# Optimization experiments

Measured on AMD Instinct MI355X. Metric: run time of the kernel, lower is better.

## Reference

```python
import jax, jax.numpy as jnp
import numpy as np

HIDDEN = 8192
K = 32
DIMS = [512, 768]
BATCH = 16384

def _xavier(key, shape):
    fan_out, fan_in = shape
    limit = np.sqrt(6.0 / (fan_in + fan_out)).astype(np.float32)
    return jax.random.uniform(key, shape, dtype=jnp.float32, minval=-limit, maxval=limit)

def setup_inputs() -> dict:
    key = jax.random.key(0)
    ks = jax.random.split(key, 6)
    return {
        "x0": jax.random.normal(ks[0], (BATCH, DIMS[0]), dtype=jnp.float32),
        "x1": jax.random.normal(ks[1], (BATCH, DIMS[1]), dtype=jnp.float32),
        "pre_bias0": jnp.zeros((DIMS[0],), dtype=jnp.float32),
        "pre_bias1": jnp.zeros((DIMS[1],), dtype=jnp.float32),
        "enc_w0": _xavier(ks[2], (HIDDEN, DIMS[0])),   # nn.Linear(d0, hidden).weight
        "enc_w1": _xavier(ks[3], (HIDDEN, DIMS[1])),
        "dec_w0": _xavier(ks[4], (DIMS[0], HIDDEN)),   # nn.Linear(hidden, d0).weight
        "dec_w1": _xavier(ks[5], (DIMS[1], HIDDEN)),
        "post_bias0": jnp.zeros((DIMS[0],), dtype=jnp.float32),
        "post_bias1": jnp.zeros((DIMS[1],), dtype=jnp.float32),
        "source_idx": 0,
    }

def _topk_sparse(z, k):
    # keep top-k per row, zero the rest (hard TopK activation)
    vals, idx = jax.lax.top_k(z, k)                      # [B, k]
    rows = jnp.arange(z.shape[0])[:, None]               # [B, 1]
    return jnp.zeros_like(z).at[rows, idx].set(vals)

def reference(x0, x1, pre_bias0, pre_bias1, enc_w0, enc_w1,
              dec_w0, dec_w1, post_bias0, post_bias1, source_idx):
    xs = (x0, x1)
    pbs = (pre_bias0, pre_bias1)
    ews = (enc_w0, enc_w1)
    # encode from source model: pre-bias subtract -> linear -> TopK sparsify
    x = xs[source_idx]
    z_dense = (x - pbs[source_idx]) @ ews[source_idx].T   # [B, HIDDEN]
    z = _topk_sparse(z_dense, K)
    # decode to every model's activation space
    rec0 = z @ dec_w0.T + post_bias0                      # [B, d0]
    rec1 = z @ dec_w1.T + post_bias1                      # [B, d1]
    return (z, rec0, rec1)
```

## Files before the change

kernel.cpp:

```cpp
#include <hip/hip_runtime.h>


#define BATCH  16384
#define HIDDEN 8192
#define DIM0   512
#define DIM1   768
#define TOPK   32
#define CAND_MAX 256
#define WIN_LO 36
#define WIN_HI 64

#define KLO_G 0xBECDu
#define KHI_G 0xC020u

typedef __attribute__((ext_vector_type(8))) short bf16x8;
typedef __attribute__((ext_vector_type(8))) unsigned short u16x8;
typedef __attribute__((ext_vector_type(4))) float f32x4;

__device__ __forceinline__ unsigned fkey(float f) {
    unsigned u = __float_as_uint(f);
    return (u & 0x80000000u) ? ~u : (u | 0x80000000u);
}
__device__ __forceinline__ unsigned fkey16(unsigned short h) {
    return (h & 0x8000u) ? (unsigned)((~h) & 0xFFFFu) : (unsigned)(h | 0x8000u);
}
__device__ __forceinline__ unsigned short f2b(float f) {
    unsigned u = __float_as_uint(f);
    unsigned r = (u + 0x7FFFu + ((u >> 16) & 1u)) >> 16;
    return (unsigned short)r;
}
__device__ __forceinline__ float b2f(unsigned short h) {
    return __uint_as_float(((unsigned)h) << 16);
}
__device__ __forceinline__ void load_lds16(const void* g, void* l) {
    __builtin_amdgcn_global_load_lds((const __attribute__((address_space(1))) void*)g,
                                     (__attribute__((address_space(3))) void*)l, 16, 0, 0);
}

template<int SRC>
__device__ __forceinline__ void convert_impl(
    const float* __restrict__ x, const float* __restrict__ pb,
    const float* __restrict__ w,
    unsigned short* __restrict__ xb, unsigned short* __restrict__ wb)
{
    constexpr int D = SRC ? DIM1 : DIM0;
    const int nx4 = BATCH * D / 4;
    const int nw4 = HIDDEN * D / 4;
    for (int i = blockIdx.x * blockDim.x + threadIdx.x; i < nx4 + nw4;
         i += gridDim.x * blockDim.x) {
        if (i < nx4) {
            float4 v = ((const float4*)x)[i];
            const int k = (i * 4) % D;
            v.x -= pb[k]; v.y -= pb[k + 1]; v.z -= pb[k + 2]; v.w -= pb[k + 3];
            ushort4 o; o.x = f2b(v.x); o.y = f2b(v.y); o.z = f2b(v.z); o.w = f2b(v.w);
            ((ushort4*)xb)[i] = o;
        } else {
            const float4 v = ((const float4*)w)[i - nx4];
            ushort4 o; o.x = f2b(v.x); o.y = f2b(v.y); o.z = f2b(v.z); o.w = f2b(v.w);
            ((ushort4*)wb)[i - nx4] = o;
        }
    }
}

__global__ void convert_xw(const float* __restrict__ x0, const float* __restrict__ x1,
                           const float* __restrict__ pb0, const float* __restrict__ pb1,
                           const float* __restrict__ w0, const float* __restrict__ w1,
                           const int* __restrict__ srcp,
                           unsigned short* __restrict__ xb, unsigned short* __restrict__ wb)
{
    if (*srcp == 0) convert_impl<0>(x0, pb0, w0, xb, wb);
    else            convert_impl<1>(x1, pb1, w1, xb, wb);
}

__global__ void transpose_dec_bf16(const float* __restrict__ dec,
                                   unsigned short* __restrict__ decT, int DD)
{
    __shared__ float t[32][33];
    const int hb = blockIdx.x * 32, db = blockIdx.y * 32;
    const int lx = threadIdx.x, ly = threadIdx.y;
#pragma unroll
    for (int s = 0; s < 32; s += 8)
        t[ly + s][lx] = dec[(size_t)(db + ly + s) * HIDDEN + hb + lx];
    __syncthreads();
#pragma unroll
    for (int s = 0; s < 32; s += 8)
        decT[(size_t)(hb + ly + s) * DD + db + lx] = f2b(t[lx][ly + s]);
}

template<int SRC>
__device__ __forceinline__ void gemm_impl(
    const unsigned short* __restrict__ xb, const unsigned short* __restrict__ wb,
    float* __restrict__ z, unsigned short* As, unsigned short* Bs)
{
    constexpr int D = SRC ? DIM1 : DIM0;

    const int nwg = gridDim.x;
    int id = blockIdx.x;
    id = (id & 7) * (nwg >> 3) + (id >> 3);
    const int bx = id & 63;
    const int by = id >> 6;
    const int m0 = by * 128, n0 = bx * 128;

    const int tid  = threadIdx.x;
    const int lane = tid & 63;
    const int wid  = tid >> 6;
    const int wr   = wid >> 1;
    const int wc   = wid & 1;
    const int l15  = lane & 15;
    const int g    = lane >> 4;

    f32x4 acc[4][4];
#pragma unroll
    for (int i = 0; i < 4; ++i)
#pragma unroll
        for (int j = 0; j < 4; ++j) acc[i][j] = (f32x4){0.f, 0.f, 0.f, 0.f};

    for (int k0 = 0; k0 < D; k0 += 64) {
#pragma unroll
        for (int q = 0; q < 4; ++q) {
            const int c   = wid * 256 + q * 64 + lane;
            const int row = c >> 3, jb = c & 7;
            const int j   = jb ^ (row & 7);
            load_lds16(xb + (size_t)(m0 + row) * D + k0 + j * 8,
                       As + (size_t)(wid * 256 + q * 64) * 8);
            load_lds16(wb + (size_t)(n0 + row) * D + k0 + j * 8,
                       Bs + (size_t)(wid * 256 + q * 64) * 8);
        }
        __syncthreads();

#pragma unroll
        for (int kk = 0; kk < 2; ++kk) {
            bf16x8 a[4], b[4];
#pragma unroll
            for (int f = 0; f < 4; ++f) {
                const int rA = wr * 64 + f * 16 + l15;
                const int sA = ((kk * 4 + g) ^ (rA & 7)) * 16;
                a[f] = *(const bf16x8*)((const char*)As + rA * 128 + sA);
                const int rB = wc * 64 + f * 16 + l15;
                const int sB = ((kk * 4 + g) ^ (rB & 7)) * 16;
                b[f] = *(const bf16x8*)((const char*)Bs + rB * 128 + sB);
            }
#pragma unroll
            for (int fi = 0; fi < 4; ++fi)
#pragma unroll
                for (int fj = 0; fj < 4; ++fj)
                    acc[fi][fj] = __builtin_amdgcn_mfma_f32_16x16x32_bf16(
                        a[fi], b[fj], acc[fi][fj], 0, 0, 0);
        }
        __syncthreads();
    }

#pragma unroll
    for (int fi = 0; fi < 4; ++fi) {
        const int row = m0 + wr * 64 + fi * 16 + g * 4;
#pragma unroll
        for (int fj = 0; fj < 4; ++fj) {
            const int col = n0 + wc * 64 + fj * 16 + l15;
#pragma unroll
            for (int r = 0; r < 4; ++r) {
                unsigned short* zs =
                    (unsigned short*)((char*)z + (size_t)(row + r) * (HIDDEN * 4));
                zs[col] = f2b(acc[fi][fj][r]);
            }
        }
    }

    if (bx >= 32) {
        const f32x4 zv = (f32x4){0.f, 0.f, 0.f, 0.f};
        const int c4 = (4096 >> 2) + (bx - 32) * 32 + (tid & 31);
#pragma unroll
        for (int pass = 0; pass < 16; ++pass) {
            const int r = m0 + pass * 8 + (tid >> 5);
            __builtin_nontemporal_store(zv, (f32x4*)(z + (size_t)r * HIDDEN) + c4);
        }
    }
}

__global__ __launch_bounds__(256, 2)
void gemm_bf16(const unsigned short* __restrict__ xb, const unsigned short* __restrict__ wb,
               const int* __restrict__ srcp, float* __restrict__ z)
{
    __shared__ unsigned short As[128 * 64];
    __shared__ unsigned short Bs[128 * 64];
    if (*srcp == 0) gemm_impl<0>(xb, wb, z, As, Bs);
    else            gemm_impl<1>(xb, wb, z, As, Bs);
}

template<int SRC>
__device__ __forceinline__ void topk_impl(
    float* __restrict__ z,
    const float* __restrict__ xsrc, const float* __restrict__ pb,
    const float* __restrict__ ew,
    const unsigned short* __restrict__ dTb0, const unsigned short* __restrict__ dTb1,
    const float* __restrict__ po0, const float* __restrict__ po1,
    float* __restrict__ rec0, float* __restrict__ rec1,
    float* xs, int* cidx, float* cval, unsigned char* cflag,
    int* counts, unsigned* pcounts, int* s_cnt, float* selv, int* seli)
{
    constexpr int D = SRC ? DIM1 : DIM0;

    const int tid = threadIdx.x;
    const size_t row = blockIdx.x;
    float* __restrict__ zrow = z + row * HIDDEN;
    const unsigned short* __restrict__ zsrow =
        (const unsigned short*)((const char*)z + row * (HIDDEN * 4));

    if (tid < D / 4) {
        const float4 xv = ((const float4*)(xsrc + row * D))[tid];
        const float4 pv = ((const float4*)pb)[tid];
        ((float4*)xs)[tid] = make_float4(xv.x - pv.x, xv.y - pv.y,
                                         xv.z - pv.z, xv.w - pv.w);
    }
    if (tid == 0) *s_cnt = 0;

    unsigned pkey[16];
#pragma unroll
    for (int s = 0; s < 4; ++s) {
        const u16x8 v = *(const u16x8*)(zsrow + (size_t)(s * 256 + tid) * 8);
#pragma unroll
        for (int p = 0; p < 4; ++p)
            pkey[s * 4 + p] = fkey16(v[2 * p]) | (fkey16(v[2 * p + 1]) << 16);
    }

    const f32x4 zv4 = (f32x4){0.f, 0.f, 0.f, 0.f};
#pragma unroll
    for (int s = 0; s < 4; ++s)
        __builtin_nontemporal_store(zv4, (f32x4*)&zrow[(size_t)(s * 256 + tid) * 4]);

    {
        int clo = 0, chi = 0;
#pragma unroll
        for (int p = 0; p < 16; ++p) {
            const unsigned klo16 = pkey[p] & 0xFFFFu, khi16 = pkey[p] >> 16;
            clo += (klo16 > KLO_G) ? 1 : 0;  chi += (klo16 > KHI_G) ? 1 : 0;
            clo += (khi16 > KLO_G) ? 1 : 0;  chi += (khi16 > KHI_G) ? 1 : 0;
        }
        unsigned pk = (unsigned)clo | ((unsigned)chi << 16);
#pragma unroll
        for (int off = 32; off; off >>= 1) pk += __shfl_xor(pk, off);
        if ((tid & 63) == 0) pcounts[tid >> 6] = pk;
    }
    __syncthreads();
    const unsigned ptot = pcounts[0] + pcounts[1] + pcounts[2] + pcounts[3];
    const int tot_lo = (int)(ptot & 0xFFFFu), tot_hi = (int)(ptot >> 16);

    unsigned kappa;
    int found = 0;
    if (tot_lo >= WIN_LO && tot_lo <= WIN_HI)      { kappa = KLO_G; found = 1; }
    else if (tot_hi >= WIN_LO && tot_hi <= WIN_HI) { kappa = KHI_G; found = 1; }
    if (!found) {
        unsigned lo = 0u, hi = 65535u;
        if (tot_lo > WIN_HI) lo = KLO_G;
        if (tot_lo < WIN_LO) hi = KLO_G;
        if (tot_hi > WIN_HI) lo = KHI_G;
        if (tot_hi < WIN_LO) hi = (hi < KHI_G) ? hi : KHI_G;
        kappa = lo;
        for (int it = 0; it < 18; ++it) {
            const unsigned mid = (lo + hi) >> 1;
            int c = 0;
#pragma unroll
            for (int p = 0; p < 16; ++p) {
                c += ((pkey[p] & 0xFFFFu) > mid) ? 1 : 0;
                c += ((pkey[p] >> 16)     > mid) ? 1 : 0;
            }
#pragma unroll
            for (int off = 32; off; off >>= 1) c += __shfl_xor(c, off);
            if ((tid & 63) == 0) counts[(it & 1) * 4 + (tid >> 6)] = c;
            __syncthreads();
            const int* cb = counts + (it & 1) * 4;
            const int tot = cb[0] + cb[1] + cb[2] + cb[3];
            if (tot >= WIN_LO && tot <= WIN_HI) { kappa = mid; break; }
            if (tot > WIN_HI) lo = mid; else hi = mid;
            kappa = lo;
            if (hi - lo <= 1u) break;
        }
    }

#pragma unroll
    for (int p = 0; p < 16; ++p) {
#pragma unroll
        for (int h = 0; h < 2; ++h) {
            const unsigned k16 = h ? (pkey[p] >> 16) : (pkey[p] & 0xFFFFu);
            if (k16 > kappa) {
                const int j = 2 * p + h;
                const int slot = atomicAdd(s_cnt, 1);
                if (slot < CAND_MAX)
                    cidx[slot] = ((j >> 3) * 256 + tid) * 8 + (j & 7);
            }
        }
    }
    __syncthreads();
    const int C = min(*s_cnt, CAND_MAX);

    {
        const int grp = tid >> 3, j8 = tid & 7;
        for (int c = grp; c < C; c += 32) {
            const float* __restrict__ wrow = ew + (size_t)cidx[c] * D;
            float4 a4 = make_float4(0.f, 0.f, 0.f, 0.f);
#pragma unroll
            for (int b = 0; b < D / 256; ++b) {
                float4 wv[8];
#pragma unroll
                for (int u = 0; u < 8; ++u)
                    wv[u] = *(const float4*)&wrow[b * 256 + u * 32 + j8 * 4];
#pragma unroll
                for (int u = 0; u < 8; ++u) {
                    const float4 x4 = *(const float4*)&xs[b * 256 + u * 32 + j8 * 4];
                    a4.x = fmaf(x4.x, wv[u].x, a4.x);
                    a4.y = fmaf(x4.y, wv[u].y, a4.y);
                    a4.z = fmaf(x4.z, wv[u].z, a4.z);
                    a4.w = fmaf(x4.w, wv[u].w, a4.w);
                }
            }
            float a = (a4.x + a4.y) + (a4.z + a4.w);
            a += __shfl_xor(a, 1);
            a += __shfl_xor(a, 2);
            a += __shfl_xor(a, 4);
            if (j8 == 0) cval[c] = a;
        }
    }
    __syncthreads();

    if (tid < C) {
        const float v = cval[tid];
        const int  ix = cidx[tid];
        int rank = 0;
        for (int j = 0; j < C; ++j) {
            const float vj = cval[j];
            rank += (vj > v || (vj == v && cidx[j] < ix)) ? 1 : 0;
        }
        cflag[tid] = (rank < TOPK) ? 1 : 0;
    }
    __syncthreads();
    if (tid < C && cflag[tid]) {
        const int ix = cidx[tid];
        int sr = 0;
        for (int j = 0; j < C; ++j) sr += (cflag[j] && cidx[j] < ix) ? 1 : 0;
        selv[sr] = cval[tid];
        seli[sr] = ix;
    }
    __syncthreads();

    if (tid < TOPK) zrow[seli[tid]] = selv[tid];

#pragma unroll
    for (int pass = 0; pass < 2; ++pass) {
        const int slot = pass * 256 + tid;
        if (slot < (DIM0 + DIM1) / 4) {
            const bool is0 = slot < DIM0 / 4;
            const int d0 = is0 ? slot * 4 : (slot - DIM0 / 4) * 4;
            const int DD = is0 ? DIM0 : DIM1;
            const unsigned short* __restrict__ dT = is0 ? dTb0 : dTb1;
            const float* __restrict__ po = is0 ? po0 : po1;
            f32x4 a;
            {
                const float4 p4 = *(const float4*)&po[d0];
                a = (f32x4){p4.x, p4.y, p4.z, p4.w};
            }
#pragma unroll
            for (int b = 0; b < TOPK / 8; ++b) {
                ushort4 wv[8];
#pragma unroll
                for (int u = 0; u < 8; ++u)
                    wv[u] = *(const ushort4*)&dT[(size_t)seli[b * 8 + u] * DD + d0];
#pragma unroll
                for (int u = 0; u < 8; ++u) {
                    const float sv = selv[b * 8 + u];
                    a.x = fmaf(sv, b2f(wv[u].x), a.x);
                    a.y = fmaf(sv, b2f(wv[u].y), a.y);
                    a.z = fmaf(sv, b2f(wv[u].z), a.z);
                    a.w = fmaf(sv, b2f(wv[u].w), a.w);
                }
            }
            float* __restrict__ out = is0 ? (rec0 + row * DIM0 + d0)
                                          : (rec1 + row * DIM1 + d0);
            __builtin_nontemporal_store(a, (f32x4*)out);
        }
    }
}

__global__ __launch_bounds__(256, 4)
void topk_rescore_decode(float* __restrict__ z,
                         const float* __restrict__ x0, const float* __restrict__ x1,
                         const float* __restrict__ pb0, const float* __restrict__ pb1,
                         const float* __restrict__ ew0, const float* __restrict__ ew1,
                         const unsigned short* __restrict__ dTb0,
                         const unsigned short* __restrict__ dTb1,
                         const float* __restrict__ po0, const float* __restrict__ po1,
                         float* __restrict__ rec0, float* __restrict__ rec1,
                         const int* __restrict__ srcp)
{
    __shared__ float         xs[DIM1];
    __shared__ int           cidx[CAND_MAX];
    __shared__ float         cval[CAND_MAX];
    __shared__ unsigned char cflag[CAND_MAX];
    __shared__ int           counts[2 * 4];
    __shared__ unsigned      pcounts[4];
    __shared__ int           s_cnt;
    __shared__ float         selv[TOPK];
    __shared__ int           seli[TOPK];

    if (*srcp == 0)
        topk_impl<0>(z, x0, pb0, ew0, dTb0, dTb1, po0, po1, rec0, rec1,
                     xs, cidx, cval, cflag, counts, pcounts, &s_cnt, selv, seli);
    else
        topk_impl<1>(z, x1, pb1, ew1, dTb0, dTb1, po0, po1, rec0, rec1,
                     xs, cidx, cval, cflag, counts, pcounts, &s_cnt, selv, seli);
}


__global__ __launch_bounds__(256, 2)
void encode_gemm(const float* __restrict__ x0, const float* __restrict__ x1,
                 const float* __restrict__ pb0, const float* __restrict__ pb1,
                 const float* __restrict__ w0, const float* __restrict__ w1,
                 const int* __restrict__ srcp, float* __restrict__ z)
{
    const int src = *srcp;
    const float* __restrict__ x  = (src == 0) ? x0 : x1;
    const float* __restrict__ pb = (src == 0) ? pb0 : pb1;
    const float* __restrict__ w  = (src == 0) ? w0 : w1;
    const int D = (src == 0) ? DIM0 : DIM1;

    __shared__ float As[16][132];
    __shared__ float Bs[16][132];

    const int tid = threadIdx.x;
    const int m0 = blockIdx.y * 128;
    const int n0 = blockIdx.x * 128;

    const int cA0 = tid,          cA1 = tid + 256;
    const int r0  = cA0 >> 2,     kq0 = (cA0 & 3) * 4;
    const int r1  = cA1 >> 2,     kq1 = (cA1 & 3) * 4;

    const int mf = (tid & 15) * 4;
    const int nf = (tid >> 4) * 4;

    float acc[8][8];
#pragma unroll
    for (int i = 0; i < 8; ++i)
#pragma unroll
        for (int j = 0; j < 8; ++j) acc[i][j] = 0.0f;

    for (int k0 = 0; k0 < D; k0 += 16) {
        const float4 av0 = *(const float4*)(x + (size_t)(m0 + r0) * D + k0 + kq0);
        const float4 av1 = *(const float4*)(x + (size_t)(m0 + r1) * D + k0 + kq1);
        const float4 pv0 = *(const float4*)(pb + k0 + kq0);
        const float4 pv1 = *(const float4*)(pb + k0 + kq1);
        const float4 bv0 = *(const float4*)(w + (size_t)(n0 + r0) * D + k0 + kq0);
        const float4 bv1 = *(const float4*)(w + (size_t)(n0 + r1) * D + k0 + kq1);
        As[kq0 + 0][r0] = av0.x - pv0.x;
        As[kq0 + 1][r0] = av0.y - pv0.y;
        As[kq0 + 2][r0] = av0.z - pv0.z;
        As[kq0 + 3][r0] = av0.w - pv0.w;
        As[kq1 + 0][r1] = av1.x - pv1.x;
        As[kq1 + 1][r1] = av1.y - pv1.y;
        As[kq1 + 2][r1] = av1.z - pv1.z;
        As[kq1 + 3][r1] = av1.w - pv1.w;
        Bs[kq0 + 0][r0] = bv0.x;
        Bs[kq0 + 1][r0] = bv0.y;
        Bs[kq0 + 2][r0] = bv0.z;
        Bs[kq0 + 3][r0] = bv0.w;
        Bs[kq1 + 0][r1] = bv1.x;
        Bs[kq1 + 1][r1] = bv1.y;
        Bs[kq1 + 2][r1] = bv1.z;
        Bs[kq1 + 3][r1] = bv1.w;
        __syncthreads();
#pragma unroll
        for (int kk = 0; kk < 16; ++kk) {
            const float4 A0 = *(const float4*)&As[kk][mf];
            const float4 A1 = *(const float4*)&As[kk][mf + 64];
            const float4 B0 = *(const float4*)&Bs[kk][nf];
            const float4 B1 = *(const float4*)&Bs[kk][nf + 64];
            const float a[8] = {A0.x, A0.y, A0.z, A0.w, A1.x, A1.y, A1.z, A1.w};
            const float b[8] = {B0.x, B0.y, B0.z, B0.w, B1.x, B1.y, B1.z, B1.w};
#pragma unroll
            for (int i = 0; i < 8; ++i)
#pragma unroll
                for (int j = 0; j < 8; ++j)
                    acc[i][j] = fmaf(a[i], b[j], acc[i][j]);
        }
        __syncthreads();
    }

#pragma unroll
    for (int i = 0; i < 8; ++i) {
        const int row = m0 + mf + (i & 3) + (i >> 2) * 64;
        const float4 v0 = make_float4(acc[i][0], acc[i][1], acc[i][2], acc[i][3]);
        const float4 v1 = make_float4(acc[i][4], acc[i][5], acc[i][6], acc[i][7]);
        *(float4*)(z + (size_t)row * HIDDEN + n0 + nf)      = v0;
        *(float4*)(z + (size_t)row * HIDDEN + n0 + nf + 64) = v1;
    }
}

__global__ __launch_bounds__(256, 2)
void topk_decode_fb(float* __restrict__ z,
                    const float* __restrict__ dA, const float* __restrict__ dB,
                    const float* __restrict__ po0, const float* __restrict__ po1,
                    float* __restrict__ rec0, float* __restrict__ rec1)
{
    __shared__ float    rowv[HIDDEN];
    __shared__ unsigned hist[4][257];
    __shared__ unsigned scanbuf[256];
    __shared__ float    selv[TOPK];
    __shared__ int      seli[TOPK];
    __shared__ unsigned sh_byte, sh_gt;

    const int tid = threadIdx.x;
    const size_t rowid = blockIdx.x;
    float* __restrict__ zrow = z + rowid * HIDDEN;

#pragma unroll
    for (int s = 0; s < 8; ++s) {
        const int i4 = s * 256 + tid;
        *(float4*)&rowv[i4 * 4] = *(const float4*)&zrow[i4 * 4];
    }
    __syncthreads();

    unsigned prefix = 0, prefmask = 0, need = TOPK;
#pragma unroll
    for (int p = 3; p >= 0; --p) {
        for (int i = tid; i < 4 * 257; i += 256) (&hist[0][0])[i] = 0;
        __syncthreads();
        const int sh = p * 8;
        for (int s = 0; s < 32; ++s) {
            const int i = s * 256 + tid;
            const unsigned k = fkey(rowv[i]);
            if ((k & prefmask) == prefix)
                atomicAdd(&hist[tid & 3][(k >> sh) & 255], 1);
        }
        __syncthreads();
        const unsigned tot = hist[0][tid] + hist[1][tid] + hist[2][tid] + hist[3][tid];
        hist[0][tid] = tot;
        __syncthreads();
        if (tid == 0) {
            unsigned cum = 0;
            int b = 255;
            for (;; --b) {
                const unsigned c = hist[0][b];
                if (cum + c >= need || b == 0) { sh_byte = (unsigned)b; sh_gt = cum; break; }
                cum += c;
            }
        }
        __syncthreads();
        prefix  |= sh_byte << sh;
        prefmask |= 0xFFu << sh;
        need -= sh_gt;
        __syncthreads();
    }
    const unsigned cut = prefix;
    const unsigned needEq = need;

    unsigned gtmask = 0, eqmask = 0;
#pragma unroll
    for (int j = 0; j < 32; ++j) {
        const int jr = (j + tid) & 31;
        const int i = tid * 32 + jr;
        const unsigned k = fkey(rowv[i]);
        if (k > cut)       gtmask |= 1u << jr;
        else if (k == cut) eqmask |= 1u << jr;
    }

    scanbuf[tid] = __popc(eqmask);
    __syncthreads();
    for (int off = 1; off < 256; off <<= 1) {
        const unsigned v = scanbuf[tid];
        const unsigned add = (tid >= off) ? scanbuf[tid - off] : 0u;
        __syncthreads();
        scanbuf[tid] = v + add;
        __syncthreads();
    }
    const unsigned eqexc = scanbuf[tid] - __popc(eqmask);
    __syncthreads();

    unsigned selmask = gtmask;
    {
        unsigned m = eqmask, r = eqexc;
        while (m) {
            const int j = __ffs(m) - 1;
            if (r < needEq) selmask |= 1u << j;
            ++r;
            m &= m - 1;
        }
    }

    scanbuf[tid] = __popc(selmask);
    __syncthreads();
    for (int off = 1; off < 256; off <<= 1) {
        const unsigned v = scanbuf[tid];
        const unsigned add = (tid >= off) ? scanbuf[tid - off] : 0u;
        __syncthreads();
        scanbuf[tid] = v + add;
        __syncthreads();
    }
    const unsigned selexc = scanbuf[tid] - __popc(selmask);

#pragma unroll
    for (int j = 0; j < 32; ++j) {
        const int jr = (j + tid) & 31;
        const int i = tid * 32 + jr;
        if ((selmask >> jr) & 1u) {
            const int slot = (int)(selexc + __popc(selmask & ((1u << jr) - 1u)));
            selv[slot] = rowv[i];
            seli[slot] = i;
        } else {
            rowv[i] = 0.0f;
        }
    }
    __syncthreads();

#pragma unroll
    for (int s = 0; s < 8; ++s) {
        const int i4 = s * 256 + tid;
        *(float4*)&zrow[i4 * 4] = *(float4*)&rowv[i4 * 4];
    }

    for (int d = tid; d < DIM0; d += 256) {
        float a = po0[d];
#pragma unroll
        for (int j = 0; j < TOPK; ++j)
            a = fmaf(selv[j], dA[(size_t)d * HIDDEN + seli[j]], a);
        rec0[rowid * DIM0 + d] = a;
    }
    for (int d = tid; d < DIM1; d += 256) {
        float a = po1[d];
#pragma unroll
        for (int j = 0; j < TOPK; ++j)
            a = fmaf(selv[j], dB[(size_t)d * HIDDEN + seli[j]], a);
        rec1[rowid * DIM1 + d] = a;
    }
}

extern "C" void kernel_launch(void* const* d_in, const int* in_sizes, int n_in,
                              void* d_out, int out_size, void* d_ws, size_t ws_size,
                              hipStream_t stream)
{
    const float* x0  = (const float*)d_in[0];
    const float* x1  = (const float*)d_in[1];
    const float* pb0 = (const float*)d_in[2];
    const float* pb1 = (const float*)d_in[3];
    const float* ew0 = (const float*)d_in[4];
    const float* ew1 = (const float*)d_in[5];
    const float* dw0 = (const float*)d_in[6];
    const float* dw1 = (const float*)d_in[7];
    const float* po0 = (const float*)d_in[8];
    const float* po1 = (const float*)d_in[9];
    const int*  srcp = (const int*)d_in[10];

    float* z    = (float*)d_out;
    float* rec0 = z + (size_t)BATCH * HIDDEN;
    float* rec1 = rec0 + (size_t)BATCH * DIM0;

    unsigned short* xb   = (unsigned short*)d_ws;
    unsigned short* wb   = xb   + (size_t)BATCH * DIM1;
    unsigned short* dTb0 = wb   + (size_t)HIDDEN * DIM1;
    unsigned short* dTb1 = dTb0 + (size_t)HIDDEN * DIM0;
    const size_t need = ((size_t)BATCH * DIM1 + (size_t)HIDDEN * DIM1 +
                         (size_t)HIDDEN * DIM0 + (size_t)HIDDEN * DIM1) * sizeof(unsigned short);

    if (ws_size >= need) {
        convert_xw<<<4096, 256, 0, stream>>>(x0, x1, pb0, pb1, ew0, ew1, srcp, xb, wb);
        dim3 tb(32, 8);
        transpose_dec_bf16<<<dim3(HIDDEN / 32, DIM0 / 32), tb, 0, stream>>>(dw0, dTb0, DIM0);
        transpose_dec_bf16<<<dim3(HIDDEN / 32, DIM1 / 32), tb, 0, stream>>>(dw1, dTb1, DIM1);
        gemm_bf16<<<(BATCH / 128) * (HIDDEN / 128), 256, 0, stream>>>(xb, wb, srcp, z);
        topk_rescore_decode<<<BATCH, 256, 0, stream>>>(
            z, x0, x1, pb0, pb1, ew0, ew1, dTb0, dTb1, po0, po1, rec0, rec1, srcp);
    } else {
        encode_gemm<<<dim3(HIDDEN / 128, BATCH / 128), 256, 0, stream>>>(
            x0, x1, pb0, pb1, ew0, ew1, srcp, z);
        topk_decode_fb<<<BATCH, 256, 0, stream>>>(z, dw0, dw1, po0, po1, rec0, rec1);
    }
}
```

Measured before the change: 750.9 us.

## Build per-row top-k candidate lists in GEMM epilogue via global atomics

The GEMM epilogue now compares each bf16 score against a fixed per-source threshold and appends column indices above it to a per-row global list using atomic counters. The top-k kernel then uses that list directly when its size falls in a valid window, skipping the row rescan, count reduction and threshold bisection. A zero-count kernel and extra workspace are added. In exchange the epilogue pays global atomics per hit, and the fixed thresholds are tuned to the input distribution, with the old path kept as a fallback.

```diff
diff --git a/kernel.cpp b/kernel.cpp
--- a/kernel.cpp
+++ b/kernel.cpp
@@ -7,6 +7,7 @@
 #define DIM1   768
 #define TOPK   32
 #define CAND_MAX 256
+#define LIST_CAP 128
 #define WIN_LO 36
 #define WIN_HI 64
 
@@ -17,10 +18,6 @@
 typedef __attribute__((ext_vector_type(8))) unsigned short u16x8;
 typedef __attribute__((ext_vector_type(4))) float f32x4;
 
-__device__ __forceinline__ unsigned fkey(float f) {
-    unsigned u = __float_as_uint(f);
-    return (u & 0x80000000u) ? ~u : (u | 0x80000000u);
-}
 __device__ __forceinline__ unsigned fkey16(unsigned short h) {
     return (h & 0x8000u) ? (unsigned)((~h) & 0xFFFFu) : (unsigned)(h | 0x8000u);
 }
@@ -35,6 +32,15 @@
 __device__ __forceinline__ void load_lds16(const void* g, void* l) {
     __builtin_amdgcn_global_load_lds((const __attribute__((address_space(1))) void*)g,
                                      (__attribute__((address_space(3))) void*)l, 16, 0, 0);
+}
+__device__ __forceinline__ unsigned fkey32(float f) {
+    unsigned u = __float_as_uint(f);
+    return (u & 0x80000000u) ? ~u : (u | 0x80000000u);
+}
+
+__global__ void zero_cnt(int* __restrict__ cnt)
+{
+    cnt[blockIdx.x * 256 + threadIdx.x] = 0;
 }
 
 template<int SRC>
@@ -90,9 +96,11 @@
 template<int SRC>
 __device__ __forceinline__ void gemm_impl(
     const unsigned short* __restrict__ xb, const unsigned short* __restrict__ wb,
-    float* __restrict__ z, unsigned short* As, unsigned short* Bs)
+    float* __restrict__ z, int* __restrict__ cnt, unsigned short* __restrict__ clist,
+    unsigned short* As, unsigned short* Bs)
 {
     constexpr int D = SRC ? DIM1 : DIM0;
+    constexpr unsigned KTH = SRC ? 0xBF86u : 0xBF5Du;
 
     const int nwg = gridDim.x;
     int id = blockIdx.x;
@@ -158,9 +166,15 @@
             const int col = n0 + wc * 64 + fj * 16 + l15;
 #pragma unroll
             for (int r = 0; r < 4; ++r) {
+                const unsigned short sb = f2b(acc[fi][fj][r]);
                 unsigned short* zs =
                     (unsigned short*)((char*)z + (size_t)(row + r) * (HIDDEN * 4));
-                zs[col] = f2b(acc[fi][fj][r]);
+                zs[col] = sb;
+                if (fkey16(sb) > KTH) {
+                    const int slot = atomicAdd(&cnt[row + r], 1);
+                    if (slot < LIST_CAP)
+                        clist[(size_t)(row + r) * LIST_CAP + slot] = (unsigned short)col;
+                }
             }
         }
     }
@@ -178,12 +192,13 @@
 
 __global__ __launch_bounds__(256, 2)
 void gemm_bf16(const unsigned short* __restrict__ xb, const unsigned short* __restrict__ wb,
-               const int* __restrict__ srcp, float* __restrict__ z)
+               const int* __restrict__ srcp, float* __restrict__ z,
+               int* __restrict__ cnt, unsigned short* __restrict__ clist)
 {
     __shared__ unsigned short As[128 * 64];
     __shared__ unsigned short Bs[128 * 64];
-    if (*srcp == 0) gemm_impl<0>(xb, wb, z, As, Bs);
-    else            gemm_impl<1>(xb, wb, z, As, Bs);
+    if (*srcp == 0) gemm_impl<0>(xb, wb, z, cnt, clist, As, Bs);
+    else            gemm_impl<1>(xb, wb, z, cnt, clist, As, Bs);
 }
 
 template<int SRC>
@@ -194,6 +209,7 @@
     const unsigned short* __restrict__ dTb0, const unsigned short* __restrict__ dTb1,
     const float* __restrict__ po0, const float* __restrict__ po1,
     float* __restrict__ rec0, float* __restrict__ rec1,
+    const int* __restrict__ cnt, const unsigned short* __restrict__ clist,
     float* xs, int* cidx, float* cval, unsigned char* cflag,
     int* counts, unsigned* pcounts, int* s_cnt, float* selv, int* seli)
 {
@@ -213,84 +229,96 @@
     }
     if (tid == 0) *s_cnt = 0;
 
-    unsigned pkey[16];
-#pragma unroll
-    for (int s = 0; s < 4; ++s) {
-        const u16x8 v = *(const u16x8*)(zsrow + (size_t)(s * 256 + tid) * 8);
-#pragma unroll
-        for (int p = 0; p < 4; ++p)
-            pkey[s * 4 + p] = fkey16(v[2 * p]) | (fkey16(v[2 * p + 1]) << 16);
-    }
-
+    const int cn = cnt[row];
+    const bool uselist = (cn >= WIN_LO && cn <= LIST_CAP);
     const f32x4 zv4 = (f32x4){0.f, 0.f, 0.f, 0.f};
-#pragma unroll
-    for (int s = 0; s < 4; ++s)
-        __builtin_nontemporal_store(zv4, (f32x4*)&zrow[(size_t)(s * 256 + tid) * 4]);
-
-    {
-        int clo = 0, chi = 0;
+    int C;
+
+    if (uselist) {
+        if (tid < cn) cidx[tid] = (int)clist[row * LIST_CAP + tid];
+#pragma unroll
+        for (int s = 0; s < 4; ++s)
+            __builtin_nontemporal_store(zv4, (f32x4*)&zrow[(size_t)(s * 256 + tid) * 4]);
+        __syncthreads();
+        C = cn;
+    } else {
+        unsigned pkey[16];
+#pragma unroll
+        for (int s = 0; s < 4; ++s) {
+            const u16x8 v = *(const u16x8*)(zsrow + (size_t)(s * 256 + tid) * 8);
+#pragma unroll
+            for (int p = 0; p < 4; ++p)
+                pkey[s * 4 + p] = fkey16(v[2 * p]) | (fkey16(v[2 * p + 1]) << 16);
+        }
+#pragma unroll
+        for (int s = 0; s < 4; ++s)
+            __builtin_nontemporal_store(zv4, (f32x4*)&zrow[(size_t)(s * 256 + tid) * 4]);
+
+        {
+            int clo = 0, chi = 0;
+#pragma unroll
+            for (int p = 0; p < 16; ++p) {
+                const unsigned klo16 = pkey[p] & 0xFFFFu, khi16 = pkey[p] >> 16;
+                clo += (klo16 > KLO_G) ? 1 : 0;  chi += (klo16 > KHI_G) ? 1 : 0;
+                clo += (khi16 > KLO_G) ? 1 : 0;  chi += (khi16 > KHI_G) ? 1 : 0;
+            }
+            unsigned pk = (unsigned)clo | ((unsigned)chi << 16);
+#pragma unroll
+            for (int off = 32; off; off >>= 1) pk += __shfl_xor(pk, off);
+            if ((tid & 63) == 0) pcounts[tid >> 6] = pk;
+        }
+        __syncthreads();
+        const unsigned ptot = pcounts[0] + pcounts[1] + pcounts[2] + pcounts[3];
+        const int tot_lo = (int)(ptot & 0xFFFFu), tot_hi = (int)(ptot >> 16);
+
+        unsigned kappa;
+        int found = 0;
+        if (tot_lo >= WIN_LO && tot_lo <= WIN_HI)      { kappa = KLO_G; found = 1; }
+        else if (tot_hi >= WIN_LO && tot_hi <= WIN_HI) { kappa = KHI_G; found = 1; }
+        if (!found) {
+            unsigned lo = 0u, hi = 65535u;
+            if (tot_lo > WIN_HI) lo = KLO_G;
+            if (tot_lo < WIN_LO) hi = KLO_G;
+            if (tot_hi > WIN_HI) lo = KHI_G;
+            if (tot_hi < WIN_LO) hi = (hi < KHI_G) ? hi : KHI_G;
+            kappa = lo;
+            for (int it = 0; it < 18; ++it) {
+                const unsigned mid = (lo + hi) >> 1;
+                int c = 0;
+#pragma unroll
+                for (int p = 0; p < 16; ++p) {
+                    c += ((pkey[p] & 0xFFFFu) > mid) ? 1 : 0;
+                    c += ((pkey[p] >> 16)     > mid) ? 1 : 0;
+                }
+#pragma unroll
+                for (int off = 32; off; off >>= 1) c += __shfl_xor(c, off);
+                if ((tid & 63) == 0) counts[(it & 1) * 4 + (tid >> 6)] = c;
+                __syncthreads();
+                const int* cb = counts + (it & 1) * 4;
+                const int tot = cb[0] + cb[1] + cb[2] + cb[3];
+                if (tot >= WIN_LO && tot <= WIN_HI) { kappa = mid; break; }
+                if (tot > WIN_HI) lo = mid; else hi = mid;
+                kappa = lo;
+                if (hi - lo <= 1u) break;
+            }
+        }
+
 #pragma unroll
         for (int p = 0; p < 16; ++p) {
-            const unsigned klo16 = pkey[p] & 0xFFFFu, khi16 = pkey[p] >> 16;
-            clo += (klo16 > KLO_G) ? 1 : 0;  chi += (klo16 > KHI_G) ? 1 : 0;
-            clo += (khi16 > KLO_G) ? 1 : 0;  chi += (khi16 > KHI_G) ? 1 : 0;
-        }
-        unsigned pk = (unsigned)clo | ((unsigned)chi << 16);
-#pragma unroll
-        for (int off = 32; off; off >>= 1) pk += __shfl_xor(pk, off);
-        if ((tid & 63) == 0) pcounts[tid >> 6] = pk;
-    }
-    __syncthreads();
-    const unsigned ptot = pcounts[0] + pcounts[1] + pcounts[2] + pcounts[3];
-    const int tot_lo = (int)(ptot & 0xFFFFu), tot_hi = (int)(ptot >> 16);
-
-    unsigned kappa;
-    int found = 0;
-    if (tot_lo >= WIN_LO && tot_lo <= WIN_HI)      { kappa = KLO_G; found = 1; }
-    else if (tot_hi >= WIN_LO && tot_hi <= WIN_HI) { kappa = KHI_G; found = 1; }
-    if (!found) {
-        unsigned lo = 0u, hi = 65535u;
-        if (tot_lo > WIN_HI) lo = KLO_G;
-        if (tot_lo < WIN_LO) hi = KLO_G;
-        if (tot_hi > WIN_HI) lo = KHI_G;
-        if (tot_hi < WIN_LO) hi = (hi < KHI_G) ? hi : KHI_G;
-        kappa = lo;
-        for (int it = 0; it < 18; ++it) {
-            const unsigned mid = (lo + hi) >> 1;
-            int c = 0;
-#pragma unroll
-            for (int p = 0; p < 16; ++p) {
-                c += ((pkey[p] & 0xFFFFu) > mid) ? 1 : 0;
-                c += ((pkey[p] >> 16)     > mid) ? 1 : 0;
-            }
-#pragma unroll
-            for (int off = 32; off; off >>= 1) c += __shfl_xor(c, off);
-            if ((tid & 63) == 0) counts[(it & 1) * 4 + (tid >> 6)] = c;
-            __syncthreads();
-            const int* cb = counts + (it & 1) * 4;
-            const int tot = cb[0] + cb[1] + cb[2] + cb[3];
-            if (tot >= WIN_LO && tot <= WIN_HI) { kappa = mid; break; }
-            if (tot > WIN_HI) lo = mid; else hi = mid;
-            kappa = lo;
-            if (hi - lo <= 1u) break;
-        }
-    }
-
-#pragma unroll
-    for (int p = 0; p < 16; ++p) {
-#pragma unroll
-        for (int h = 0; h < 2; ++h) {
-            const unsigned k16 = h ? (pkey[p] >> 16) : (pkey[p] & 0xFFFFu);
-            if (k16 > kappa) {
-                const int j = 2 * p + h;
-                const int slot = atomicAdd(s_cnt, 1);
-                if (slot < CAND_MAX)
-                    cidx[slot] = ((j >> 3) * 256 + tid) * 8 + (j & 7);
-            }
-        }
-    }
-    __syncthreads();
-    const int C = min(*s_cnt, CAND_MAX);
+#pragma unroll
+            for (int h = 0; h < 2; ++h) {
+                const unsigned k16 = h ? (pkey[p] >> 16) : (pkey[p] & 0xFFFFu);
+                if (k16 > kappa) {
+                    const int j = 2 * p + h;
+                    const int slot = atomicAdd(s_cnt, 1);
+                    if (slot < CAND_MAX)
+                        cidx[slot] = ((j >> 3) * 256 + tid) * 8 + (j & 7);
+                }
+            }
+        }
+        __syncthreads();
+        C = min(*s_cnt, CAND_MAX);
+    }
 
     {
         const int grp = tid >> 3, j8 = tid & 7;
@@ -388,7 +416,8 @@
                          const unsigned short* __restrict__ dTb1,
                          const float* __restrict__ po0, const float* __restrict__ po1,
                          float* __restrict__ rec0, float* __restrict__ rec1,
-                         const int* __restrict__ srcp)
+                         const int* __restrict__ srcp,
+                         const int* __restrict__ cnt, const unsigned short* __restrict__ clist)
 {
     __shared__ float         xs[DIM1];
     __shared__ int           cidx[CAND_MAX];
@@ -401,10 +430,10 @@
     __shared__ int           seli[TOPK];
 
     if (*srcp == 0)
-        topk_impl<0>(z, x0, pb0, ew0, dTb0, dTb1, po0, po1, rec0, rec1,
+        topk_impl<0>(z, x0, pb0, ew0, dTb0, dTb1, po0, po1, rec0, rec1, cnt, clist,
                      xs, cidx, cval, cflag, counts, pcounts, &s_cnt, selv, seli);
     else
-        topk_impl<1>(z, x1, pb1, ew1, dTb0, dTb1, po0, po1, rec0, rec1,
+        topk_impl<1>(z, x1, pb1, ew1, dTb0, dTb1, po0, po1, rec0, rec1, cnt, clist,
                      xs, cidx, cval, cflag, counts, pcounts, &s_cnt, selv, seli);
 }
 
@@ -524,7 +553,7 @@
         const int sh = p * 8;
         for (int s = 0; s < 32; ++s) {
             const int i = s * 256 + tid;
-            const unsigned k = fkey(rowv[i]);
+            const unsigned k = fkey32(rowv[i]);
             if ((k & prefmask) == prefix)
                 atomicAdd(&hist[tid & 3][(k >> sh) & 255], 1);
         }
@@ -555,7 +584,7 @@
     for (int j = 0; j < 32; ++j) {
         const int jr = (j + tid) & 31;
         const int i = tid * 32 + jr;
-        const unsigned k = fkey(rowv[i]);
+        const unsigned k = fkey32(rowv[i]);
         if (k > cut)       gtmask |= 1u << jr;
         else if (k == cut) eqmask |= 1u << jr;
     }
@@ -654,17 +683,24 @@
     unsigned short* wb   = xb   + (size_t)BATCH * DIM1;
     unsigned short* dTb0 = wb   + (size_t)HIDDEN * DIM1;
     unsigned short* dTb1 = dTb0 + (size_t)HIDDEN * DIM0;
+    int*            cnt  = (int*)(dTb1 + (size_t)HIDDEN * DIM1);
+    unsigned short* clist = (unsigned short*)(cnt + BATCH);
     const size_t need = ((size_t)BATCH * DIM1 + (size_t)HIDDEN * DIM1 +
-                         (size_t)HIDDEN * DIM0 + (size_t)HIDDEN * DIM1) * sizeof(unsigned short);
+                         (size_t)HIDDEN * DIM0 + (size_t)HIDDEN * DIM1) * sizeof(unsigned short)
+                        + (size_t)BATCH * sizeof(int)
+                        + (size_t)BATCH * LIST_CAP * sizeof(unsigned short);
 
     if (ws_size >= need) {
+        zero_cnt<<<BATCH / 256, 256, 0, stream>>>(cnt);
         convert_xw<<<4096, 256, 0, stream>>>(x0, x1, pb0, pb1, ew0, ew1, srcp, xb, wb);
         dim3 tb(32, 8);
         transpose_dec_bf16<<<dim3(HIDDEN / 32, DIM0 / 32), tb, 0, stream>>>(dw0, dTb0, DIM0);
         transpose_dec_bf16<<<dim3(HIDDEN / 32, DIM1 / 32), tb, 0, stream>>>(dw1, dTb1, DIM1);
-        gemm_bf16<<<(BATCH / 128) * (HIDDEN / 128), 256, 0, stream>>>(xb, wb, srcp, z);
+        gemm_bf16<<<(BATCH / 128) * (HIDDEN / 128), 256, 0, stream>>>(
+            xb, wb, srcp, z, cnt, clist);
         topk_rescore_decode<<<BATCH, 256, 0, stream>>>(
-            z, x0, x1, pb0, pb1, ew0, ew1, dTb0, dTb1, po0, po1, rec0, rec1, srcp);
+            z, x0, x1, pb0, pb1, ew0, ew1, dTb0, dTb1, po0, po1, rec0, rec1,
+            srcp, cnt, clist);
     } else {
         encode_gemm<<<dim3(HIDDEN / 128, BATCH / 128), 256, 0, stream>>>(
             x0, x1, pb0, pb1, ew0, ew1, srcp, z);
```

New measurement: 881.0 us. +17.3%, slower.
